# Optimization experiments

Measured on AMD Instinct MI355X. Metric: run time of the kernel, lower is better.

## Reference

```python
import jax, jax.numpy as jnp
import numpy as np

NEG_INF = -1e9  # matches masked_fill value -1000000000.0
LEAKY_SLOPE = 0.2


def setup_inputs() -> dict:
    key = jax.random.key(0)
    k1, k2, k3, k4 = jax.random.split(key, 4)
    B, N, D_in, D_out = 8, 2048, 256, 256
    x = jax.random.normal(k1, (B, N, D_in), dtype=jnp.float32)
    adj_matrix = jax.random.randint(k2, (B, N, N), 0, 2, dtype=jnp.int32)
    # torch nn.Linear weights: W is [out, in], attention a is [1, 2*out]
    W = jax.random.normal(k3, (D_out, D_in), dtype=jnp.float32) / np.sqrt(D_in)
    a = jax.random.normal(k4, (1, 2 * D_out), dtype=jnp.float32) / np.sqrt(2 * D_out)
    return {"x": x, "adj_matrix": adj_matrix, "W": W, "a": a}


def reference(x, adj_matrix, W, a):
    # h = W(x): [B, N, D_out]
    h = jnp.einsum('bnd,od->bno', x, W)
    D = h.shape[-1]
    # attention(concat(h_i, h_j)) == h_i @ a_left + h_j @ a_right (bias-free linear)
    a_left, a_right = a[0, :D], a[0, D:]
    e = (h @ a_left)[:, :, None] + (h @ a_right)[:, None, :]  # [B, N, N]
    e = jnp.where(e > 0, e, LEAKY_SLOPE * e)  # LeakyReLU(0.2)
    e = jnp.where(adj_matrix == 0, NEG_INF, e)
    alpha = jax.nn.softmax(e, axis=-1)
    return jnp.einsum('bij,bjd->bid', alpha, h)
```

## Files before the change

### kernel.cpp

```cpp
#include <hip/hip_runtime.h>
#include <hip/hip_bf16.h>

typedef __attribute__((ext_vector_type(8))) __bf16 bf16x8;
typedef __attribute__((ext_vector_type(4))) float f32x4;
typedef __attribute__((ext_vector_type(4))) int int4v;

#define NB 8
#define NN 2048
#define ND 256
#define L2E 1.44269504f
#define AS1 __attribute__((address_space(1)))
#define AS3 __attribute__((address_space(3)))

__global__ __launch_bounds__(256) void k5_pack(
    const int* __restrict__ adj, unsigned long long* __restrict__ mask) {
  const long NSEG = (long)NB * NN * (NN / 64);
  int lane = threadIdx.x & 63;
  long gw = (((long)blockIdx.x * 256 + threadIdx.x) >> 6);
  long stride = ((long)gridDim.x * 256) >> 6;
  for (long s = gw; s < NSEG; s += stride) {
    int v = adj[s * 64 + lane];
    unsigned long long m = __ballot(v != 0);
    if (lane == 0) mask[s] = m;
  }
}

__global__ __launch_bounds__(256) void k2_elr(
    const float* __restrict__ x, const float* __restrict__ W,
    const float* __restrict__ a, float* __restrict__ elc,
    float* __restrict__ er2) {
  __shared__ float wls[ND], wrs[ND];
  int t = threadIdx.x;
  {
    float swl = 0.f, swr = 0.f;
    for (int o = 0; o < ND; ++o) {
      float wv = W[(long)o * ND + t];
      swl = fmaf(a[o], wv, swl);
      swr = fmaf(a[ND + o], wv, swr);
    }
    wls[t] = swl;
    wrs[t] = swr;
  }
  __syncthreads();
  int r = t >> 2, q = t & 3;
  long row = (long)blockIdx.x * 64 + r;
  const f32x4* xr = (const f32x4*)(x + row * ND);
  float sl = 0.f, sr = 0.f;
#pragma unroll
  for (int ii = 0; ii < 16; ++ii) {
    int idx = q + (ii << 2);
    f32x4 xv = xr[idx];
    f32x4 lv = *(const f32x4*)(wls + idx * 4);
    f32x4 rv = *(const f32x4*)(wrs + idx * 4);
    sl += xv[0] * lv[0] + xv[1] * lv[1] + xv[2] * lv[2] + xv[3] * lv[3];
    sr += xv[0] * rv[0] + xv[1] * rv[1] + xv[2] * rv[2] + xv[3] * rv[3];
  }
  sl += __shfl_xor(sl, 1);
  sl += __shfl_xor(sl, 2);
  sr += __shfl_xor(sr, 1);
  sr += __shfl_xor(sr, 2);
  if (q == 0) {
    elc[row] = (-0.8f * sl - 16.0f) * L2E;
    float2 v;
    v.x = (sr - 16.0f) * L2E;
    v.y = 0.2f * sr * L2E;
    *(float2*)(er2 + row * 2) = v;
  }
}

__global__ __launch_bounds__(256) void k1_h(
    const float* __restrict__ x, const float* __restrict__ W,
    __bf16* __restrict__ hT2) {
  __shared__ __bf16 hlds[256 * 34];
  int tid = threadIdx.x;
  int wid = tid >> 6, lane = tid & 63;
  int msub = wid & 1, nh = wid >> 1;
  int lrow = lane & 15, kg = lane >> 4;
  int m0 = blockIdx.x * 32;
  int row = m0 + msub * 16 + lrow;

  f32x4 acc[8];
#pragma unroll
  for (int f = 0; f < 8; ++f) acc[f] = (f32x4){0.f, 0.f, 0.f, 0.f};

#pragma unroll
  for (int k0 = 0; k0 < ND; k0 += 32) {
    int kk = k0 + kg * 8;
    const f32x4* xa = (const f32x4*)(x + (long)row * ND + kk);
    f32x4 a0 = xa[0], a1 = xa[1];
    bf16x8 afrag;
    afrag[0] = (__bf16)a0[0]; afrag[1] = (__bf16)a0[1];
    afrag[2] = (__bf16)a0[2]; afrag[3] = (__bf16)a0[3];
    afrag[4] = (__bf16)a1[0]; afrag[5] = (__bf16)a1[1];
    afrag[6] = (__bf16)a1[2]; afrag[7] = (__bf16)a1[3];
#pragma unroll
    for (int f = 0; f < 8; ++f) {
      int o = nh * 128 + f * 16 + lrow;
      const f32x4* wb = (const f32x4*)(W + (long)o * ND + kk);
      f32x4 b0 = wb[0], b1 = wb[1];
      bf16x8 bfrag;
      bfrag[0] = (__bf16)b0[0]; bfrag[1] = (__bf16)b0[1];
      bfrag[2] = (__bf16)b0[2]; bfrag[3] = (__bf16)b0[3];
      bfrag[4] = (__bf16)b1[0]; bfrag[5] = (__bf16)b1[1];
      bfrag[6] = (__bf16)b1[2]; bfrag[7] = (__bf16)b1[3];
      acc[f] = __builtin_amdgcn_mfma_f32_16x16x32_bf16(afrag, bfrag, acc[f], 0, 0, 0);
    }
  }

#pragma unroll
  for (int f = 0; f < 8; ++f) {
    int d = nh * 128 + f * 16 + lrow;
#pragma unroll
    for (int r = 0; r < 4; ++r) {
      int nloc = msub * 16 + kg * 4 + r;
      hlds[d * 34 + nloc] = (__bf16)acc[f][r];
    }
  }
  __syncthreads();
  {
    int b = m0 >> 11;
    int jc = (m0 & (NN - 1)) >> 5;
    const int* src = (const int*)(hlds + tid * 34);
    int tmp[16];
#pragma unroll
    for (int j = 0; j < 16; ++j) tmp[j] = src[j];
    __bf16* dst = hT2 + (((long)b * 64 + jc) * 256 + tid) * 32;
#pragma unroll
    for (int j = 0; j < 4; ++j)
      *(int4v*)(dst + j * 8) = *(int4v*)(tmp + j * 4);
  }
}

__global__ __launch_bounds__(512, 4) void k3_main(
    const unsigned* __restrict__ mask32, const __bf16* __restrict__ hT2,
    const float* __restrict__ elc, const float* __restrict__ er2,
    float* __restrict__ out) {
  __shared__ __bf16 hbuf[3][8192];
  __shared__ float er_lds[NN * 2];
  __shared__ unsigned mask_lds[32 * 65];

  int blk = blockIdx.x;
  int b = blk & 7;
  int it = blk >> 3;
  int tid = threadIdx.x;
  int wid = tid >> 6, lane = tid & 63;
  int isub = wid & 1, dh = wid >> 1;
  int lrow = lane & 15, kg = lane >> 4;
  int irow = it * 32 + isub * 16 + lrow;

  const __bf16* hT2b = hT2 + (long)b * 64 * 8192;
  const unsigned* maskb = mask32 + ((long)b * NN + (long)it * 32) * 64;
  const float* er2b = er2 + (long)b * NN * 2;
  float c1s = elc[b * NN + irow];
  int kg8 = kg * 8;

  int4v mw = *(const int4v*)(maskb + tid * 4);
  __builtin_amdgcn_global_load_lds((const AS1 void*)(er2b + tid * 4),
                                   (AS3 void*)(er_lds + tid * 4), 16, 0, 0);
  __builtin_amdgcn_global_load_lds((const AS1 void*)(er2b + 2048 + tid * 4),
                                   (AS3 void*)(er_lds + 2048 + tid * 4), 16, 0, 0);

  int d0 = tid >> 2, slot = tid & 3;
  int jlog = slot ^ ((d0 >> 1) & 3);
  const __bf16* sgbase = hT2b + d0 * 32 + jlog * 8;

#define STAGEH(BI, TCV)                                                      \
  {                                                                          \
    const __bf16* s_ = sgbase + (long)(TCV)*8192;                            \
    __builtin_amdgcn_global_load_lds((const AS1 void*)(s_),                  \
                                     (AS3 void*)(&hbuf[BI][tid * 8]), 16, 0, 0); \
    __builtin_amdgcn_global_load_lds(                                        \
        (const AS1 void*)(s_ + 4096),                                        \
        (AS3 void*)(&hbuf[BI][4096 + tid * 8]), 16, 0, 0);                   \
  }

  STAGEH(0, 0);
  STAGEH(1, 1);

  asm volatile("s_waitcnt vmcnt(6)" ::: "memory");
  {
    int mrow = tid >> 4, mcol = (tid & 15) * 4;
    *(int4v*)(mask_lds + mrow * 65 + mcol) = mw;
  }
  asm volatile("s_waitcnt lgkmcnt(0)" ::: "memory");
  __builtin_amdgcn_s_barrier();

  int hoff = (dh * 64 + lrow) * 64 + (kg ^ ((lrow >> 1) & 3)) * 16;
  int d_base = dh * 64 + lrow;
  int mbase = (isub * 16 + lrow) * 65;

  f32x4 acc[4];
#pragma unroll
  for (int f = 0; f < 4; ++f) acc[f] = (f32x4){0.f, 0.f, 0.f, 0.f};
  float den = 0.f;

#define COMPUTE(BI, TCV)                                                     \
  {                                                                          \
    unsigned msh = mask_lds[mbase + (TCV)] >> kg8;                           \
    const float* ep_ = er_lds + ((TCV)*32 + kg8) * 2;                        \
    f32x4 e0 = *(const f32x4*)(ep_);                                         \
    f32x4 e1 = *(const f32x4*)(ep_ + 4);                                     \
    f32x4 e2 = *(const f32x4*)(ep_ + 8);                                     \
    f32x4 e3 = *(const f32x4*)(ep_ + 12);                                    \
    bf16x8 pfrag;                                                            \
    float ps = 0.f;                                                          \
    _Pragma("unroll") for (int e = 0; e < 8; ++e) {                          \
      f32x4 ev = (e < 2) ? e0 : (e < 4) ? e1 : (e < 6) ? e2 : e3;            \
      float x16 = ev[(e & 1) * 2];                                           \
      float x02 = ev[(e & 1) * 2 + 1];                                       \
      float m = fmaxf(x16, x02 + c1s);                                       \
      float p = __builtin_amdgcn_exp2f(m);                                   \
      p = ((msh >> e) & 1u) ? p : 0.0f;                                      \
      ps += p;                                                               \
      pfrag[e] = (__bf16)p;                                                  \
    }                                                                        \
    den += ps;                                                               \
    const char* hb = (const char*)&hbuf[BI][0];                              \
    __builtin_amdgcn_s_setprio(1);                                           \
    _Pragma("unroll") for (int f = 0; f < 4; ++f) {                          \
      bf16x8 bfr = *(const bf16x8*)(hb + hoff + f * 1024);                   \
      acc[f] = __builtin_amdgcn_mfma_f32_16x16x32_bf16(pfrag, bfr, acc[f], 0, 0, 0); \
    }                                                                        \
    __builtin_amdgcn_s_setprio(0);                                           \
  }

#define WAITB(VMN)                                       \
  asm volatile("s_waitcnt vmcnt(" VMN ")" ::: "memory"); \
  __builtin_amdgcn_s_barrier();

  for (int t3 = 0; t3 < 20; ++t3) {
    int tc = t3 * 3;
    WAITB("2"); STAGEH(2, tc + 2); COMPUTE(0, tc);
    WAITB("2"); STAGEH(0, tc + 3); COMPUTE(1, tc + 1);
    WAITB("2"); STAGEH(1, tc + 4); COMPUTE(2, tc + 2);
  }
  WAITB("2"); STAGEH(2, 62); COMPUTE(0, 60);
  WAITB("2"); STAGEH(0, 63); COMPUTE(1, 61);
  WAITB("2"); COMPUTE(2, 62);
  WAITB("0"); COMPUTE(0, 63);

#undef STAGEH
#undef COMPUTE
#undef WAITB

  den += __shfl_xor(den, 16);
  den += __shfl_xor(den, 32);
  float rdiv[4];
#pragma unroll
  for (int r = 0; r < 4; ++r) rdiv[r] = 1.0f / __shfl(den, kg * 4 + r);

  float* outb = out + ((long)b * NN + it * 32 + isub * 16) * ND;
#pragma unroll
  for (int f = 0; f < 4; ++f) {
    int dcol = d_base + f * 16;
#pragma unroll
    for (int r = 0; r < 4; ++r)
      outb[(long)(kg * 4 + r) * ND + dcol] = acc[f][r] * rdiv[r];
  }
}

extern "C" void kernel_launch(void* const* d_in, const int* in_sizes, int n_in,
                              void* d_out, int out_size, void* d_ws,
                              size_t ws_size, hipStream_t stream) {
  const float* x = (const float*)d_in[0];
  const int* adj = (const int*)d_in[1];
  const float* W = (const float*)d_in[2];
  const float* a = (const float*)d_in[3];
  float* out = (float*)d_out;

  char* ws = (char*)d_ws;
  const size_t base = 8u * 1024u * 1024u;
  __bf16* hT2 = (__bf16*)ws;
  float* elc = (float*)(ws + base);
  float* er2 = (float*)(ws + base + 65536u);
  unsigned long long* mask =
      (unsigned long long*)(ws + base + 262144u);

  k5_pack<<<dim3(2048), dim3(256), 0, stream>>>(adj, mask);
  k1_h<<<dim3(512), dim3(256), 0, stream>>>(x, W, hT2);
  k2_elr<<<dim3(256), dim3(256), 0, stream>>>(x, W, a, elc, er2);
  k3_main<<<dim3(512), dim3(512), 0, stream>>>((const unsigned*)mask, hT2, elc,
                                               er2, out);
}
```

Before: 131.7 us.

## Fuse prep kernels into one launch and deepen main-loop LDS pipeline

Merges the mask-packing, h projection and attention-logit kernels into a single launch, with blocks dispatched by index range, so two launch gaps disappear and the independent work can overlap. The main kernel moves from a 3-buffer to a 4-buffer LDS ring for h tiles, giving each load more time in flight. It also stores only one er value per node and recomputes the second with an FMA, halving that LDS table. The mask table drops its padded stride for an XOR swizzle to avoid bank conflicts. The extra LDS buffer may lower occupancy, and the fused prep kernel carries the largest shared-memory footprint of its branches for every block.

Result: slower. 157.8 us (+19.8%).

```diff
diff --git a/kernel.cpp b/kernel.cpp
--- a/kernel.cpp
+++ b/kernel.cpp
@@ -12,71 +12,71 @@
 #define AS1 __attribute__((address_space(1)))
 #define AS3 __attribute__((address_space(3)))
 
-__global__ __launch_bounds__(256) void k5_pack(
-    const int* __restrict__ adj, unsigned long long* __restrict__ mask) {
-  const long NSEG = (long)NB * NN * (NN / 64);
-  int lane = threadIdx.x & 63;
-  long gw = (((long)blockIdx.x * 256 + threadIdx.x) >> 6);
-  long stride = ((long)gridDim.x * 256) >> 6;
-  for (long s = gw; s < NSEG; s += stride) {
-    int v = adj[s * 64 + lane];
-    unsigned long long m = __ballot(v != 0);
-    if (lane == 0) mask[s] = m;
-  }
-}
-
-__global__ __launch_bounds__(256) void k2_elr(
+__global__ __launch_bounds__(256) void kprep(
     const float* __restrict__ x, const float* __restrict__ W,
-    const float* __restrict__ a, float* __restrict__ elc,
-    float* __restrict__ er2) {
+    const float* __restrict__ a, const int* __restrict__ adj,
+    __bf16* __restrict__ hT2, float* __restrict__ elc,
+    float* __restrict__ erx, unsigned long long* __restrict__ mask) {
+  __shared__ __bf16 hlds[256 * 34];
   __shared__ float wls[ND], wrs[ND];
-  int t = threadIdx.x;
-  {
-    float swl = 0.f, swr = 0.f;
-    for (int o = 0; o < ND; ++o) {
-      float wv = W[(long)o * ND + t];
-      swl = fmaf(a[o], wv, swl);
-      swr = fmaf(a[ND + o], wv, swr);
-    }
-    wls[t] = swl;
-    wrs[t] = swr;
-  }
-  __syncthreads();
-  int r = t >> 2, q = t & 3;
-  long row = (long)blockIdx.x * 64 + r;
-  const f32x4* xr = (const f32x4*)(x + row * ND);
-  float sl = 0.f, sr = 0.f;
-#pragma unroll
-  for (int ii = 0; ii < 16; ++ii) {
-    int idx = q + (ii << 2);
-    f32x4 xv = xr[idx];
-    f32x4 lv = *(const f32x4*)(wls + idx * 4);
-    f32x4 rv = *(const f32x4*)(wrs + idx * 4);
-    sl += xv[0] * lv[0] + xv[1] * lv[1] + xv[2] * lv[2] + xv[3] * lv[3];
-    sr += xv[0] * rv[0] + xv[1] * rv[1] + xv[2] * rv[2] + xv[3] * rv[3];
-  }
-  sl += __shfl_xor(sl, 1);
-  sl += __shfl_xor(sl, 2);
-  sr += __shfl_xor(sr, 1);
-  sr += __shfl_xor(sr, 2);
-  if (q == 0) {
-    elc[row] = (-0.8f * sl - 16.0f) * L2E;
-    float2 v;
-    v.x = (sr - 16.0f) * L2E;
-    v.y = 0.2f * sr * L2E;
-    *(float2*)(er2 + row * 2) = v;
-  }
-}
-
-__global__ __launch_bounds__(256) void k1_h(
-    const float* __restrict__ x, const float* __restrict__ W,
-    __bf16* __restrict__ hT2) {
-  __shared__ __bf16 hlds[256 * 34];
+  int blk = blockIdx.x;
   int tid = threadIdx.x;
+
+  if (blk >= 768) {
+    const long NSEG = (long)NB * NN * (NN / 64);
+    int lane = tid & 63;
+    long gw = ((long)(blk - 768) * 256 + tid) >> 6;
+    long stride = (2048L * 256) >> 6;
+    for (long s = gw; s < NSEG; s += stride) {
+      int v = adj[s * 64 + lane];
+      unsigned long long m = __ballot(v != 0);
+      if (lane == 0) mask[s] = m;
+    }
+    return;
+  }
+
+  if (blk >= 512) {
+    int t = tid;
+    {
+      float swl = 0.f, swr = 0.f;
+#pragma unroll 8
+      for (int o = 0; o < ND; ++o) {
+        float wv = W[(long)o * ND + t];
+        swl = fmaf(a[o], wv, swl);
+        swr = fmaf(a[ND + o], wv, swr);
+      }
+      wls[t] = swl;
+      wrs[t] = swr;
+    }
+    __syncthreads();
+    int r = t >> 2, q = t & 3;
+    long row = (long)(blk - 512) * 64 + r;
+    const f32x4* xr = (const f32x4*)(x + row * ND);
+    float sl = 0.f, sr = 0.f;
+#pragma unroll
+    for (int ii = 0; ii < 16; ++ii) {
+      int idx = q + (ii << 2);
+      f32x4 xv = xr[idx];
+      f32x4 lv = *(const f32x4*)(wls + idx * 4);
+      f32x4 rv = *(const f32x4*)(wrs + idx * 4);
+      sl += xv[0] * lv[0] + xv[1] * lv[1] + xv[2] * lv[2] + xv[3] * lv[3];
+      sr += xv[0] * rv[0] + xv[1] * rv[1] + xv[2] * rv[2] + xv[3] * rv[3];
+    }
+    sl += __shfl_xor(sl, 1);
+    sl += __shfl_xor(sl, 2);
+    sr += __shfl_xor(sr, 1);
+    sr += __shfl_xor(sr, 2);
+    if (q == 0) {
+      elc[row] = (-0.8f * sl - 16.0f) * L2E;
+      erx[row] = (sr - 16.0f) * L2E;
+    }
+    return;
+  }
+
   int wid = tid >> 6, lane = tid & 63;
   int msub = wid & 1, nh = wid >> 1;
   int lrow = lane & 15, kg = lane >> 4;
-  int m0 = blockIdx.x * 32;
+  int m0 = blk * 32;
   int row = m0 + msub * 16 + lrow;
 
   f32x4 acc[8];
@@ -133,11 +133,11 @@
 
 __global__ __launch_bounds__(512, 4) void k3_main(
     const unsigned* __restrict__ mask32, const __bf16* __restrict__ hT2,
-    const float* __restrict__ elc, const float* __restrict__ er2,
+    const float* __restrict__ elc, const float* __restrict__ erx,
     float* __restrict__ out) {
-  __shared__ __bf16 hbuf[3][8192];
-  __shared__ float er_lds[NN * 2];
-  __shared__ unsigned mask_lds[32 * 65];
+  __shared__ __bf16 hbuf[4][8192];
+  __shared__ float er_lds[NN];
+  __shared__ unsigned mask_lds[2048];
 
   int blk = blockIdx.x;
   int b = blk & 7;
@@ -145,99 +145,100 @@
   int tid = threadIdx.x;
   int wid = tid >> 6, lane = tid & 63;
   int isub = wid & 1, dh = wid >> 1;
-  int lrow = lane & 15, kg = lane >> 4;
+  int lrow = lane & 15, kg = lane >> 4, kg8 = kg * 8;
   int irow = it * 32 + isub * 16 + lrow;
 
   const __bf16* hT2b = hT2 + (long)b * 64 * 8192;
   const unsigned* maskb = mask32 + ((long)b * NN + (long)it * 32) * 64;
-  const float* er2b = er2 + (long)b * NN * 2;
+  const float* erxb = erx + (long)b * NN;
   float c1s = elc[b * NN + irow];
-  int kg8 = kg * 8;
-
-  int4v mw = *(const int4v*)(maskb + tid * 4);
-  __builtin_amdgcn_global_load_lds((const AS1 void*)(er2b + tid * 4),
+
+  __builtin_amdgcn_global_load_lds((const AS1 void*)(erxb + tid * 4),
                                    (AS3 void*)(er_lds + tid * 4), 16, 0, 0);
-  __builtin_amdgcn_global_load_lds((const AS1 void*)(er2b + 2048 + tid * 4),
-                                   (AS3 void*)(er_lds + 2048 + tid * 4), 16, 0, 0);
 
   int d0 = tid >> 2, slot = tid & 3;
   int jlog = slot ^ ((d0 >> 1) & 3);
   const __bf16* sgbase = hT2b + d0 * 32 + jlog * 8;
 
-#define STAGEH(BI, TCV)                                                      \
-  {                                                                          \
-    const __bf16* s_ = sgbase + (long)(TCV)*8192;                            \
-    __builtin_amdgcn_global_load_lds((const AS1 void*)(s_),                  \
+#define STAGEH(BI, TCV)                                                       \
+  {                                                                           \
+    const __bf16* s_ = sgbase + (long)(TCV)*8192;                             \
+    __builtin_amdgcn_global_load_lds((const AS1 void*)(s_),                   \
                                      (AS3 void*)(&hbuf[BI][tid * 8]), 16, 0, 0); \
-    __builtin_amdgcn_global_load_lds(                                        \
-        (const AS1 void*)(s_ + 4096),                                        \
-        (AS3 void*)(&hbuf[BI][4096 + tid * 8]), 16, 0, 0);                   \
+    __builtin_amdgcn_global_load_lds(                                         \
+        (const AS1 void*)(s_ + 4096),                                         \
+        (AS3 void*)(&hbuf[BI][4096 + tid * 8]), 16, 0, 0);                    \
   }
 
   STAGEH(0, 0);
   STAGEH(1, 1);
-
-  asm volatile("s_waitcnt vmcnt(6)" ::: "memory");
+  STAGEH(2, 2);
+  int4v mw = *(const int4v*)(maskb + tid * 4);
+
+  asm volatile("s_waitcnt vmcnt(0)" ::: "memory");
   {
-    int mrow = tid >> 4, mcol = (tid & 15) * 4;
-    *(int4v*)(mask_lds + mrow * 65 + mcol) = mw;
+    int R = tid >> 4;
+    int w0 = (tid & 15) * 4;
+#pragma unroll
+    for (int i = 0; i < 4; ++i)
+      mask_lds[R * 64 + ((w0 + i) ^ (R & 31))] = (unsigned)mw[i];
   }
   asm volatile("s_waitcnt lgkmcnt(0)" ::: "memory");
   __builtin_amdgcn_s_barrier();
 
   int hoff = (dh * 64 + lrow) * 64 + (kg ^ ((lrow >> 1) & 3)) * 16;
   int d_base = dh * 64 + lrow;
-  int mbase = (isub * 16 + lrow) * 65;
+  int mrow = isub * 16 + lrow;
+  int mbase = mrow * 64;
+  int mxor = mrow & 31;
 
   f32x4 acc[4];
 #pragma unroll
   for (int f = 0; f < 4; ++f) acc[f] = (f32x4){0.f, 0.f, 0.f, 0.f};
   float den = 0.f;
 
-#define COMPUTE(BI, TCV)                                                     \
-  {                                                                          \
-    unsigned msh = mask_lds[mbase + (TCV)] >> kg8;                           \
-    const float* ep_ = er_lds + ((TCV)*32 + kg8) * 2;                        \
-    f32x4 e0 = *(const f32x4*)(ep_);                                         \
-    f32x4 e1 = *(const f32x4*)(ep_ + 4);                                     \
-    f32x4 e2 = *(const f32x4*)(ep_ + 8);                                     \
-    f32x4 e3 = *(const f32x4*)(ep_ + 12);                                    \
-    bf16x8 pfrag;                                                            \
-    float ps = 0.f;                                                          \
-    _Pragma("unroll") for (int e = 0; e < 8; ++e) {                          \
-      f32x4 ev = (e < 2) ? e0 : (e < 4) ? e1 : (e < 6) ? e2 : e3;            \
-      float x16 = ev[(e & 1) * 2];                                           \
-      float x02 = ev[(e & 1) * 2 + 1];                                       \
-      float m = fmaxf(x16, x02 + c1s);                                       \
-      float p = __builtin_amdgcn_exp2f(m);                                   \
-      p = ((msh >> e) & 1u) ? p : 0.0f;                                      \
-      ps += p;                                                               \
-      pfrag[e] = (__bf16)p;                                                  \
-    }                                                                        \
-    den += ps;                                                               \
-    const char* hb = (const char*)&hbuf[BI][0];                              \
-    __builtin_amdgcn_s_setprio(1);                                           \
-    _Pragma("unroll") for (int f = 0; f < 4; ++f) {                          \
-      bf16x8 bfr = *(const bf16x8*)(hb + hoff + f * 1024);                   \
+#define COMPUTE(BI, TCV)                                                      \
+  {                                                                           \
+    unsigned msh = mask_lds[mbase + ((TCV) ^ mxor)] >> kg8;                   \
+    const float* ep_ = er_lds + (TCV)*32 + kg8;                               \
+    f32x4 xa_ = *(const f32x4*)ep_;                                           \
+    f32x4 xb_ = *(const f32x4*)(ep_ + 4);                                     \
+    bf16x8 pfrag;                                                             \
+    float ps = 0.f;                                                           \
+    _Pragma("unroll") for (int e = 0; e < 8; ++e) {                           \
+      float x16 = (e < 4) ? xa_[e] : xb_[e - 4];                              \
+      float x02 = fmaf(0.2f, x16, 4.61662413f);                               \
+      float m_ = fmaxf(x16, x02 + c1s);                                       \
+      float p = __builtin_amdgcn_exp2f(m_);                                   \
+      p = ((msh >> e) & 1u) ? p : 0.0f;                                       \
+      ps += p;                                                                \
+      pfrag[e] = (__bf16)p;                                                   \
+    }                                                                         \
+    den += ps;                                                                \
+    const char* hb_ = (const char*)&hbuf[BI][0];                              \
+    __builtin_amdgcn_s_setprio(1);                                            \
+    _Pragma("unroll") for (int f = 0; f < 4; ++f) {                           \
+      bf16x8 bfr = *(const bf16x8*)(hb_ + hoff + f * 1024);                   \
       acc[f] = __builtin_amdgcn_mfma_f32_16x16x32_bf16(pfrag, bfr, acc[f], 0, 0, 0); \
-    }                                                                        \
-    __builtin_amdgcn_s_setprio(0);                                           \
+    }                                                                         \
+    __builtin_amdgcn_s_setprio(0);                                            \
   }
 
 #define WAITB(VMN)                                       \
   asm volatile("s_waitcnt vmcnt(" VMN ")" ::: "memory"); \
   __builtin_amdgcn_s_barrier();
 
-  for (int t3 = 0; t3 < 20; ++t3) {
-    int tc = t3 * 3;
-    WAITB("2"); STAGEH(2, tc + 2); COMPUTE(0, tc);
-    WAITB("2"); STAGEH(0, tc + 3); COMPUTE(1, tc + 1);
-    WAITB("2"); STAGEH(1, tc + 4); COMPUTE(2, tc + 2);
-  }
-  WAITB("2"); STAGEH(2, 62); COMPUTE(0, 60);
-  WAITB("2"); STAGEH(0, 63); COMPUTE(1, 61);
+  for (int T = 0; T < 15; ++T) {
+    int tc = T * 4;
+    WAITB("4"); STAGEH(3, tc + 3); COMPUTE(0, tc);
+    WAITB("4"); STAGEH(0, tc + 4); COMPUTE(1, tc + 1);
+    WAITB("4"); STAGEH(1, tc + 5); COMPUTE(2, tc + 2);
+    WAITB("4"); STAGEH(2, tc + 6); COMPUTE(3, tc + 3);
+  }
+  WAITB("4"); STAGEH(3, 63); COMPUTE(0, 60);
+  WAITB("4"); COMPUTE(1, 61);
   WAITB("2"); COMPUTE(2, 62);
-  WAITB("0"); COMPUTE(0, 63);
+  WAITB("0"); COMPUTE(3, 63);
 
 #undef STAGEH
 #undef COMPUTE
@@ -272,13 +273,12 @@
   const size_t base = 8u * 1024u * 1024u;
   __bf16* hT2 = (__bf16*)ws;
   float* elc = (float*)(ws + base);
-  float* er2 = (float*)(ws + base + 65536u);
+  float* erx = (float*)(ws + base + 65536u);
   unsigned long long* mask =
-      (unsigned long long*)(ws + base + 262144u);
-
-  k5_pack<<<dim3(2048), dim3(256), 0, stream>>>(adj, mask);
-  k1_h<<<dim3(512), dim3(256), 0, stream>>>(x, W, hT2);
-  k2_elr<<<dim3(256), dim3(256), 0, stream>>>(x, W, a, elc, er2);
+      (unsigned long long*)(ws + base + 131072u);
+
+  kprep<<<dim3(2816), dim3(256), 0, stream>>>(x, W, a, adj, hT2, elc, erx,
+                                              mask);
   k3_main<<<dim3(512), dim3(512), 0, stream>>>((const unsigned*)mask, hT2, elc,
-                                               er2, out);
+                                               erx, out);
 }
```
